# Performance work log

Measured on AMD Instinct MI355X. Metric: run time of the kernel, lower is better.

Reference implementation:

```python
import jax, jax.numpy as jnp
import numpy as np

B, C, H, W = 4, 256, 64, 64
CI = C // 2  # inter_channels


def setup_inputs() -> dict:
    key = jax.random.key(0)
    ks = jax.random.split(key, 10)
    s_in = 1.0 / np.sqrt(C)
    s_out = 1.0 / np.sqrt(CI)
    return {
        "rgbd": jax.random.normal(ks[0], (B, C, H, W), jnp.float32),
        "x": jax.random.normal(ks[1], (B, C, H, W), jnp.float32),
        "q_w": jax.random.uniform(ks[2], (CI, C), jnp.float32, -s_in, s_in),
        "q_b": jax.random.uniform(ks[3], (CI,), jnp.float32, -s_in, s_in),
        "k_w": jax.random.uniform(ks[4], (CI, C), jnp.float32, -s_in, s_in),
        "k_b": jax.random.uniform(ks[5], (CI,), jnp.float32, -s_in, s_in),
        "v_w": jax.random.uniform(ks[6], (CI, C), jnp.float32, -s_in, s_in),
        "v_b": jax.random.uniform(ks[7], (CI,), jnp.float32, -s_in, s_in),
        "out_w": jax.random.uniform(ks[8], (C, CI), jnp.float32, -s_out, s_out),
        "out_b": jax.random.uniform(ks[9], (C,), jnp.float32, -s_out, s_out),
    }


def reference(rgbd, x, q_w, q_b, k_w, k_b, v_w, v_b, out_w, out_b):
    b, c, h, w = rgbd.shape
    ci = q_w.shape[0]
    n = h * w
    # 1x1 convs == channel-wise linear maps; flatten spatial to tokens
    xs = x.reshape(b, c, n)        # [B, C, N]
    rs = rgbd.reshape(b, c, n)     # [B, C, N]
    q = jnp.einsum('oc,bcn->bno', q_w, xs) + q_b          # [B, N, CI]
    k = jnp.einsum('oc,bcn->bon', k_w, rs) + k_b[:, None]  # [B, CI, N]
    v = jnp.einsum('oc,bcn->bno', v_w, rs) + v_b          # [B, N, CI]
    attn = jax.nn.softmax(jnp.einsum('bqc,bck->bqk', q, k), axis=-1)  # [B, N, N]
    out = jnp.einsum('bqk,bkc->bqc', attn, v)             # [B, N, CI]
    out = jnp.einsum('oc,bnc->bon', out_w, out) + out_b[:, None]  # [B, C, N]
    return rgbd + out.reshape(b, c, h, w)
```

## Files before the change

### kernel.cpp

```cpp
#include <hip/hip_runtime.h>
#include <cstdint>
#include <cstddef>

typedef unsigned short u16;
typedef __attribute__((ext_vector_type(8))) short bf16x8;
typedef __attribute__((ext_vector_type(4))) float f32x4;

#define DEV __device__ __forceinline__

static constexpr float LOG2E = 1.4426950408889634f;

DEV u16 f2bf(float f) {
  uint32_t u = __float_as_uint(f);
  u += 0x7fffu + ((u >> 16) & 1u);
  return (u16)(u >> 16);
}
DEV float bf2f(u16 h) {
  uint32_t u = ((uint32_t)h) << 16;
  return __uint_as_float(u);
}
DEV uint32_t cvtpk(float lo, float hi) {
  uint32_t r;
  asm("v_cvt_pk_bf16_f32 %0, %1, %2" : "=v"(r) : "v"(lo), "v"(hi));
  return r;
}
DEV float exp2fast(float x) {
  float r;
  asm("v_exp_f32 %0, %1" : "=v"(r) : "v"(x));
  return r;
}

DEV f32x4 mfma16(bf16x8 a, bf16x8 b, f32x4 c) {
  return __builtin_amdgcn_mfma_f32_16x16x32_bf16(a, b, c, 0, 0, 0);
}

DEV void gload_lds16(const void* g, void* l) {
  __builtin_amdgcn_global_load_lds(
      (const __attribute__((address_space(1))) uint32_t*)g,
      (__attribute__((address_space(3))) uint32_t*)l, 16, 0, 0);
}

static constexpr int BATCH = 4;
static constexpr int C = 256;
static constexpr int CI = 128;
static constexpr int N = 4096;
static constexpr int SPLIT = 4;
static constexpr int KPB = N / SPLIT;
static constexpr int NT = KPB / 32;

__global__ __launch_bounds__(256) void cvt_w(const float* __restrict__ a,
                                             const float* __restrict__ b,
                                             const float* __restrict__ c,
                                             const float* __restrict__ d,
                                             u16* __restrict__ oa, u16* __restrict__ ob,
                                             u16* __restrict__ oc, u16* __restrict__ od) {
  int i = blockIdx.x * 256 + threadIdx.x;
  oa[i] = f2bf(a[i] * LOG2E);
  ob[i] = f2bf(b[i]);
  oc[i] = f2bf(c[i]);
  od[i] = f2bf(d[i]);
}

__global__ __launch_bounds__(256) void proj_kernel(
    const float* __restrict__ x, const float* __restrict__ rgbd,
    const u16* __restrict__ Wq, const u16* __restrict__ Wk, const u16* __restrict__ Wv,
    const float* __restrict__ qb, const float* __restrict__ kb, const float* __restrict__ vb,
    u16* __restrict__ Qb, u16* __restrict__ Kb, u16* __restrict__ Vtb) {
  __shared__ __align__(16) u16 xT[64][C + 8];
  __shared__ __align__(16) u16 rT[64][C + 8];
  const int b = blockIdx.y;
  const int n0 = blockIdx.x * 64;
  const int t = threadIdx.x;
  {
    const int tok = t & 63, cp = (t >> 6) * 2;
    const float* xb = x + (size_t)b * C * N + n0;
    const float* rb = rgbd + (size_t)b * C * N + n0;
    for (int c0 = 0; c0 < C; c0 += 8) {
      int c = c0 + cp;
      *(uint32_t*)&xT[tok][c] = cvtpk(xb[(size_t)c * N + tok], xb[(size_t)(c + 1) * N + tok]);
      *(uint32_t*)&rT[tok][c] = cvtpk(rb[(size_t)c * N + tok], rb[(size_t)(c + 1) * N + tok]);
    }
  }
  __syncthreads();
  const int w = t >> 6, lane = t & 63, g = lane >> 4, cl = lane & 15;

#define PROJ_QK(Sarr, W, bias, Out, SCL)                                              \
  {                                                                                   \
    bf16x8 afr[8];                                                                    \
    _Pragma("unroll") for (int ks = 0; ks < 8; ++ks)                                  \
        afr[ks] = *(const bf16x8*)&Sarr[w * 16 + cl][ks * 32 + g * 8];                \
    _Pragma("unroll") for (int ct = 0; ct < 8; ++ct) {                                \
      f32x4 acc = {0.f, 0.f, 0.f, 0.f};                                               \
      _Pragma("unroll") for (int ks = 0; ks < 8; ++ks) {                              \
        bf16x8 bb = *(const bf16x8*)&W[(size_t)(ct * 16 + cl) * C + ks * 32 + g * 8]; \
        acc = mfma16(afr[ks], bb, acc);                                               \
      }                                                                               \
      float bv = bias[ct * 16 + cl] * (SCL);                                          \
      _Pragma("unroll") for (int r = 0; r < 4; ++r) {                                 \
        int tok = n0 + w * 16 + g * 4 + r;                                            \
        Out[((size_t)b * N + tok) * CI + ct * 16 + cl] = f2bf(acc[r] + bv);           \
      }                                                                               \
    }                                                                                 \
  }

  PROJ_QK(xT, Wq, qb, Qb, LOG2E)
  PROJ_QK(rT, Wk, kb, Kb, 1.0f)
#undef PROJ_QK

  #pragma unroll
  for (int rt = 0; rt < 2; ++rt) {
    bf16x8 aw[8];
    #pragma unroll
    for (int ks = 0; ks < 8; ++ks)
      aw[ks] = *(const bf16x8*)&Wv[(size_t)(w * 32 + rt * 16 + cl) * C + ks * 32 + g * 8];
    #pragma unroll
    for (int ct = 0; ct < 4; ++ct) {
      f32x4 acc = {0.f, 0.f, 0.f, 0.f};
      #pragma unroll
      for (int ks = 0; ks < 8; ++ks) {
        bf16x8 bb = *(const bf16x8*)&rT[ct * 16 + cl][ks * 32 + g * 8];
        acc = mfma16(aw[ks], bb, acc);
      }
      #pragma unroll
      for (int r = 0; r < 4; ++r) {
        int o = w * 32 + rt * 16 + g * 4 + r;
        Vtb[((size_t)b * CI + o) * N + n0 + ct * 16 + cl] = f2bf(acc[r] + vb[o]);
      }
    }
  }
}

__global__ __launch_bounds__(256, 4) void attn_kernel(
    const u16* __restrict__ Qb, const u16* __restrict__ Kb,
    const u16* __restrict__ Vtb, u16* __restrict__ Opart,
    float2* __restrict__ ml) {
  __shared__ __align__(16) u16 Klds[2][32 * 128];
  __shared__ __align__(16) u16 Vlds[2][128 * 32];
  __shared__ __align__(16) u16 Plds[4][16][40];
  const int lin = blockIdx.x;
  const int nl = (lin & 7) * 128 + (lin >> 3);
  const int qi = nl & 63;
  const int grp = nl >> 6;
  const int b = grp & 3;
  const int s = grp >> 2;
  const int q0 = qi * 64;
  const int t = threadIdx.x;
  const int w = t >> 6, lane = t & 63, g = lane >> 4, cl = lane & 15;

  const u16* Kg = Kb + (size_t)b * N * CI;
  const u16* Vg = Vtb + (size_t)b * CI * N;

  const int k_r = t >> 4;
  const int k_ss = (t & 15) ^ k_r;
  const int v_r = t >> 2;
  const int v_ss = (t & 3) ^ ((t >> 4) & 3);
  const int wbase = (t & ~63);

#define STAGE_K(bi, k0_)                                                          \
  do {                                                                            \
    _Pragma("unroll") for (int c = 0; c < 2; ++c) {                               \
      gload_lds16(Kg + (size_t)((k0_) + c * 16 + k_r) * CI + k_ss * 8,            \
                  &Klds[bi][(c * 256 + wbase) * 8]);                              \
    }                                                                             \
  } while (0)
#define STAGE_V(bi, k0_)                                                          \
  do {                                                                            \
    _Pragma("unroll") for (int c = 0; c < 2; ++c) {                               \
      gload_lds16(Vg + (size_t)(c * 64 + v_r) * N + (k0_) + v_ss * 8,             \
                  &Vlds[bi][(c * 256 + wbase) * 8]);                              \
    }                                                                             \
  } while (0)

  const u16* Qg = Qb + ((size_t)b * N + q0 + w * 16 + cl) * CI;
  bf16x8 qf[4];
  #pragma unroll
  for (int ks = 0; ks < 4; ++ks)
    qf[ks] = *(const bf16x8*)(Qg + ks * 32 + g * 8);
  asm volatile("s_waitcnt vmcnt(0)" ::: "memory");

  f32x4 oacc[8];
  #pragma unroll
  for (int i = 0; i < 8; ++i) oacc[i] = {0.f, 0.f, 0.f, 0.f};
  float m = -1e30f, l = 0.f;

  const int kbeg = s * KPB;
  STAGE_K(0, kbeg);
  STAGE_V(0, kbeg);
  STAGE_K(1, kbeg + 32);
  STAGE_V(1, kbeg + 32);

  int buf = 0;
  for (int tt = 0; tt < NT; ++tt) {
    asm volatile("s_waitcnt vmcnt(4)" ::: "memory");
    __builtin_amdgcn_s_barrier();
    const int knext = kbeg + ((tt + 2 < NT) ? tt + 2 : tt) * 32;

    bf16x8 kf0[4], kf1[4];
    #pragma unroll
    for (int ks = 0; ks < 4; ++ks) {
      kf0[ks] = *(const bf16x8*)&Klds[buf][(cl)*128 + (((ks * 4 + g) ^ cl) & 15) * 8];
      kf1[ks] = *(const bf16x8*)&Klds[buf][(16 + cl) * 128 + (((ks * 4 + g) ^ cl) & 15) * 8];
    }
    asm volatile("s_waitcnt lgkmcnt(0)" ::: "memory");
    __builtin_amdgcn_s_barrier();
    STAGE_K(buf, knext);

    f32x4 st0 = {0.f, 0.f, 0.f, 0.f}, st1 = {0.f, 0.f, 0.f, 0.f};
    __builtin_amdgcn_s_setprio(1);
    #pragma unroll
    for (int ks = 0; ks < 4; ++ks) {
      st0 = mfma16(kf0[ks], qf[ks], st0);
      st1 = mfma16(kf1[ks], qf[ks], st1);
    }
    __builtin_amdgcn_s_setprio(0);

    float tmax = st0[0];
    #pragma unroll
    for (int r = 0; r < 4; ++r) tmax = fmaxf(tmax, st0[r]);
    #pragma unroll
    for (int r = 0; r < 4; ++r) tmax = fmaxf(tmax, st1[r]);
    tmax = fmaxf(tmax, __shfl_xor(tmax, 16));
    tmax = fmaxf(tmax, __shfl_xor(tmax, 32));
    if (!__all(tmax - m <= 11.5f)) {
      const float mn = fmaxf(m, tmax);
      const float alpha = exp2fast(m - mn);
      m = mn;
      l *= alpha;
      #pragma unroll
      for (int r = 0; r < 4; ++r) {
        float ar = __shfl(alpha, g * 4 + r);
        #pragma unroll
        for (int ct2 = 0; ct2 < 8; ++ct2) oacc[ct2][r] *= ar;
      }
    }
    float ls = 0.f;
    {
      float p0 = exp2fast(st0[0] - m), p1 = exp2fast(st0[1] - m);
      float p2 = exp2fast(st0[2] - m), p3 = exp2fast(st0[3] - m);
      ls += (p0 + p1) + (p2 + p3);
      *(uint32_t*)&Plds[w][cl][g * 4] = cvtpk(p0, p1);
      *(uint32_t*)&Plds[w][cl][g * 4 + 2] = cvtpk(p2, p3);
      p0 = exp2fast(st1[0] - m); p1 = exp2fast(st1[1] - m);
      p2 = exp2fast(st1[2] - m); p3 = exp2fast(st1[3] - m);
      ls += (p0 + p1) + (p2 + p3);
      *(uint32_t*)&Plds[w][cl][16 + g * 4] = cvtpk(p0, p1);
      *(uint32_t*)&Plds[w][cl][16 + g * 4 + 2] = cvtpk(p2, p3);
    }
    ls += __shfl_xor(ls, 16);
    ls += __shfl_xor(ls, 32);
    l += ls;
    bf16x8 pa = *(const bf16x8*)&Plds[w][cl][g * 8];

    bf16x8 vf[8];
    #pragma unroll
    for (int ct2 = 0; ct2 < 8; ++ct2)
      vf[ct2] = *(const bf16x8*)&Vlds[buf][(ct2 * 16 + cl) * 32 + ((g ^ (cl >> 2)) & 3) * 8];
    asm volatile("s_waitcnt lgkmcnt(0)" ::: "memory");
    __builtin_amdgcn_s_barrier();
    STAGE_V(buf, knext);

    __builtin_amdgcn_s_setprio(1);
    #pragma unroll
    for (int ct2 = 0; ct2 < 8; ++ct2)
      oacc[ct2] = mfma16(pa, vf[ct2], oacc[ct2]);
    __builtin_amdgcn_s_setprio(0);

    buf ^= 1;
  }
#undef STAGE_K
#undef STAGE_V

  #pragma unroll
  for (int r = 0; r < 4; ++r) {
    float lr = __shfl(l, g * 4 + r);
    float inv = 1.0f / lr;
    const int q = q0 + w * 16 + g * 4 + r;
    #pragma unroll
    for (int ct2 = 0; ct2 < 8; ++ct2)
      Opart[(((size_t)(s * BATCH + b)) * N + q) * CI + ct2 * 16 + cl] =
          f2bf(oacc[ct2][r] * inv);
  }
  if (g == 0) {
    const int q = q0 + w * 16 + cl;
    ml[(size_t)(s * BATCH + b) * N + q] = make_float2(m, l);
  }
}

template <int NS>
__global__ __launch_bounds__(256) void combine_kernel(
    const u16* __restrict__ Opart, const float2* __restrict__ ml,
    u16* __restrict__ Ob) {
  const int idx = blockIdx.x * 256 + threadIdx.x;
  const int ci8 = idx & 15;
  const int row = idx >> 4;
  float2 sv[NS];
  float M = -1e30f;
  #pragma unroll
  for (int sp = 0; sp < NS; ++sp) {
    sv[sp] = ml[(size_t)sp * BATCH * N + row];
    M = fmaxf(M, sv[sp].x);
  }
  float wv[NS], wsum = 0.f;
  #pragma unroll
  for (int sp = 0; sp < NS; ++sp) {
    wv[sp] = sv[sp].y * exp2fast(sv[sp].x - M);
    wsum += wv[sp];
  }
  const float invL = 1.0f / wsum;
  float acc[8];
  #pragma unroll
  for (int j = 0; j < 8; ++j) acc[j] = 0.f;
  #pragma unroll
  for (int sp = 0; sp < NS; ++sp) {
    const float ws = wv[sp] * invL;
    bf16x8 v = *(const bf16x8*)&Opart[((size_t)sp * BATCH * N + row) * CI + ci8 * 8];
    #pragma unroll
    for (int j = 0; j < 8; ++j) acc[j] += ws * bf2f((u16)v[j]);
  }
  bf16x8 o;
  #pragma unroll
  for (int j = 0; j < 8; ++j) o[j] = (short)f2bf(acc[j]);
  *(bf16x8*)&Ob[(size_t)row * CI + ci8 * 8] = o;
}

__global__ __launch_bounds__(256) void outproj_kernel(
    const u16* __restrict__ Ob, const u16* __restrict__ Wo,
    const float* __restrict__ obias, const float* __restrict__ rgbd,
    float* __restrict__ out) {
  const int b = blockIdx.y;
  const int n0 = blockIdx.x * 64;
  const int t = threadIdx.x;
  const int w = t >> 6, lane = t & 63, g = lane >> 4, cl = lane & 15;

  f32x4 acc[4][4];
  #pragma unroll
  for (int i = 0; i < 4; ++i)
    #pragma unroll
    for (int j = 0; j < 4; ++j) acc[i][j] = {0.f, 0.f, 0.f, 0.f};

  #pragma unroll
  for (int ks = 0; ks < 4; ++ks) {
    bf16x8 bo[4];
    #pragma unroll
    for (int ct = 0; ct < 4; ++ct)
      bo[ct] = *(const bf16x8*)&Ob[((size_t)b * N + n0 + ct * 16 + cl) * CI + ks * 32 + g * 8];
    #pragma unroll
    for (int rt = 0; rt < 4; ++rt) {
      bf16x8 aw = *(const bf16x8*)&Wo[(size_t)(w * 64 + rt * 16 + cl) * CI + ks * 32 + g * 8];
      #pragma unroll
      for (int ct = 0; ct < 4; ++ct) acc[rt][ct] = mfma16(aw, bo[ct], acc[rt][ct]);
    }
  }
  #pragma unroll
  for (int rt = 0; rt < 4; ++rt) {
    #pragma unroll
    for (int r = 0; r < 4; ++r) {
      const int o = w * 64 + rt * 16 + g * 4 + r;
      const float bb = obias[o];
      #pragma unroll
      for (int ct = 0; ct < 4; ++ct) {
        size_t idx = ((size_t)b * C + o) * N + n0 + ct * 16 + cl;
        out[idx] = rgbd[idx] + bb + acc[rt][ct][r];
      }
    }
  }
}

extern "C" void kernel_launch(void* const* d_in, const int* in_sizes, int n_in,
                              void* d_out, int out_size, void* d_ws, size_t ws_size,
                              hipStream_t stream) {
  (void)in_sizes; (void)n_in; (void)out_size; (void)ws_size;
  const float* rgbd = (const float*)d_in[0];
  const float* x    = (const float*)d_in[1];
  const float* q_w  = (const float*)d_in[2];
  const float* q_b  = (const float*)d_in[3];
  const float* k_w  = (const float*)d_in[4];
  const float* k_b  = (const float*)d_in[5];
  const float* v_w  = (const float*)d_in[6];
  const float* v_b  = (const float*)d_in[7];
  const float* o_w  = (const float*)d_in[8];
  const float* o_b  = (const float*)d_in[9];
  float* out = (float*)d_out;

  char* ws = (char*)d_ws;
  const size_t MB = 1024 * 1024;
  const size_t szQKV = (size_t)BATCH * N * CI * sizeof(u16);
  u16* Qb  = (u16*)(ws);
  u16* Kb  = (u16*)(ws + szQKV);
  u16* Vtb = (u16*)(ws + 2 * szQKV);
  u16* Wq  = (u16*)(ws + 3 * szQKV);
  u16* Wk  = Wq + (size_t)CI * C;
  u16* Wv  = Wk + (size_t)CI * C;
  u16* Wo  = Wv + (size_t)CI * C;
  u16* Opart = (u16*)(ws + 13 * MB);
  float2* ml = (float2*)(ws + 29 * MB);
  u16* Ob  = Qb;

  const int grid_attn = 64 * BATCH * SPLIT;

  cvt_w<<<dim3((C * CI) / 256), 256, 0, stream>>>(q_w, k_w, v_w, o_w, Wq, Wk, Wv, Wo);
  proj_kernel<<<dim3(N / 64, BATCH), 256, 0, stream>>>(x, rgbd, Wq, Wk, Wv,
                                                       q_b, k_b, v_b, Qb, Kb, Vtb);
  attn_kernel<<<dim3(grid_attn), 256, 0, stream>>>(Qb, Kb, Vtb, Opart, ml);
  combine_kernel<SPLIT><<<dim3(BATCH * N * (CI / 8) / 256), 256, 0, stream>>>(Opart, ml, Ob);
  outproj_kernel<<<dim3(N / 64, BATCH), 256, 0, stream>>>(Ob, Wo, o_b, rgbd, out);
}
```

Baseline: 106.6 us.

## Switch attention to 32x32x16 MFMA with register-resident P via permlane swap

Rewrites the flash-attention inner loop to use 32x32x16 bf16 MFMAs, with each wave owning 32 queries instead of 16. The block's query tile grows from 64 to 128 and the grid halves. Probabilities are packed and rearranged into the A operand in registers with v_permlane32_swap, removing the per-tile LDS round trip for P. This also halves K/V LDS traffic per query. The cost is more registers per thread (occupancy hint lowered from 4 to 2 blocks per CU) and fewer blocks to fill the GPU.

```diff
diff --git a/kernel.cpp b/kernel.cpp
--- a/kernel.cpp
+++ b/kernel.cpp
@@ -5,6 +5,8 @@
 typedef unsigned short u16;
 typedef __attribute__((ext_vector_type(8))) short bf16x8;
 typedef __attribute__((ext_vector_type(4))) float f32x4;
+typedef __attribute__((ext_vector_type(16))) float f32x16;
+typedef __attribute__((ext_vector_type(4))) uint32_t u32x4;
 
 #define DEV __device__ __forceinline__
 
@@ -29,9 +31,15 @@
   asm("v_exp_f32 %0, %1" : "=v"(r) : "v"(x));
   return r;
 }
+DEV void plswap(uint32_t& a, uint32_t& b) {
+  asm("v_permlane32_swap_b32 %0, %1" : "+v"(a), "+v"(b));
+}
 
 DEV f32x4 mfma16(bf16x8 a, bf16x8 b, f32x4 c) {
   return __builtin_amdgcn_mfma_f32_16x16x32_bf16(a, b, c, 0, 0, 0);
+}
+DEV f32x16 mfma32(bf16x8 a, bf16x8 b, f32x16 c) {
+  return __builtin_amdgcn_mfma_f32_32x32x16_bf16(a, b, c, 0, 0, 0);
 }
 
 DEV void gload_lds16(const void* g, void* l) {
@@ -130,22 +138,22 @@
   }
 }
 
-__global__ __launch_bounds__(256, 4) void attn_kernel(
+__global__ __launch_bounds__(256, 2) void attn_kernel(
     const u16* __restrict__ Qb, const u16* __restrict__ Kb,
     const u16* __restrict__ Vtb, u16* __restrict__ Opart,
     float2* __restrict__ ml) {
   __shared__ __align__(16) u16 Klds[2][32 * 128];
   __shared__ __align__(16) u16 Vlds[2][128 * 32];
-  __shared__ __align__(16) u16 Plds[4][16][40];
   const int lin = blockIdx.x;
-  const int nl = (lin & 7) * 128 + (lin >> 3);
-  const int qi = nl & 63;
-  const int grp = nl >> 6;
+  const int nl = (lin & 7) * 64 + (lin >> 3);
+  const int qi = nl & 31;
+  const int grp = nl >> 5;
   const int b = grp & 3;
   const int s = grp >> 2;
-  const int q0 = qi * 64;
+  const int q0 = qi * 128;
   const int t = threadIdx.x;
-  const int w = t >> 6, lane = t & 63, g = lane >> 4, cl = lane & 15;
+  const int w = t >> 6, lane = t & 63;
+  const int hi = lane >> 5, l31 = lane & 31;
 
   const u16* Kg = Kb + (size_t)b * N * CI;
   const u16* Vg = Vtb + (size_t)b * CI * N;
@@ -153,7 +161,7 @@
   const int k_r = t >> 4;
   const int k_ss = (t & 15) ^ k_r;
   const int v_r = t >> 2;
-  const int v_ss = (t & 3) ^ ((t >> 4) & 3);
+  const int v_ss = (t & 3) ^ ((t >> 3) & 3);
   const int wbase = (t & ~63);
 
 #define STAGE_K(bi, k0_)                                                          \
@@ -171,17 +179,19 @@
     }                                                                             \
   } while (0)
 
-  const u16* Qg = Qb + ((size_t)b * N + q0 + w * 16 + cl) * CI;
-  bf16x8 qf[4];
-  #pragma unroll
-  for (int ks = 0; ks < 4; ++ks)
-    qf[ks] = *(const bf16x8*)(Qg + ks * 32 + g * 8);
+  const u16* Qg = Qb + ((size_t)b * N + q0 + w * 32 + l31) * CI;
+  bf16x8 qf[8];
+  #pragma unroll
+  for (int mm = 0; mm < 8; ++mm)
+    qf[mm] = *(const bf16x8*)(Qg + mm * 16 + hi * 8);
   asm volatile("s_waitcnt vmcnt(0)" ::: "memory");
 
-  f32x4 oacc[8];
-  #pragma unroll
-  for (int i = 0; i < 8; ++i) oacc[i] = {0.f, 0.f, 0.f, 0.f};
-  float m = -1e30f, l = 0.f;
+  f32x16 oacc[4];
+  #pragma unroll
+  for (int ct = 0; ct < 4; ++ct)
+    #pragma unroll
+    for (int i = 0; i < 16; ++i) oacc[ct][i] = 0.f;
+  float m_run = -1e30f, l_run = 0.f;
 
   const int kbeg = s * KPB;
   STAGE_K(0, kbeg);
@@ -195,94 +205,101 @@
     __builtin_amdgcn_s_barrier();
     const int knext = kbeg + ((tt + 2 < NT) ? tt + 2 : tt) * 32;
 
-    bf16x8 kf0[4], kf1[4];
-    #pragma unroll
-    for (int ks = 0; ks < 4; ++ks) {
-      kf0[ks] = *(const bf16x8*)&Klds[buf][(cl)*128 + (((ks * 4 + g) ^ cl) & 15) * 8];
-      kf1[ks] = *(const bf16x8*)&Klds[buf][(16 + cl) * 128 + (((ks * 4 + g) ^ cl) & 15) * 8];
-    }
+    bf16x8 kf[8];
+    #pragma unroll
+    for (int mm = 0; mm < 8; ++mm)
+      kf[mm] = *(const bf16x8*)&Klds[buf][l31 * 128 + ((((mm << 1) | hi) ^ l31) & 15) * 8];
     asm volatile("s_waitcnt lgkmcnt(0)" ::: "memory");
     __builtin_amdgcn_s_barrier();
     STAGE_K(buf, knext);
 
-    f32x4 st0 = {0.f, 0.f, 0.f, 0.f}, st1 = {0.f, 0.f, 0.f, 0.f};
+    f32x16 st;
+    #pragma unroll
+    for (int i = 0; i < 16; ++i) st[i] = 0.f;
     __builtin_amdgcn_s_setprio(1);
     #pragma unroll
-    for (int ks = 0; ks < 4; ++ks) {
-      st0 = mfma16(kf0[ks], qf[ks], st0);
-      st1 = mfma16(kf1[ks], qf[ks], st1);
-    }
+    for (int mm = 0; mm < 8; ++mm) st = mfma32(kf[mm], qf[mm], st);
     __builtin_amdgcn_s_setprio(0);
 
-    float tmax = st0[0];
-    #pragma unroll
-    for (int r = 0; r < 4; ++r) tmax = fmaxf(tmax, st0[r]);
-    #pragma unroll
-    for (int r = 0; r < 4; ++r) tmax = fmaxf(tmax, st1[r]);
-    tmax = fmaxf(tmax, __shfl_xor(tmax, 16));
+    float tmax = st[0];
+    #pragma unroll
+    for (int i = 1; i < 16; ++i) tmax = fmaxf(tmax, st[i]);
     tmax = fmaxf(tmax, __shfl_xor(tmax, 32));
-    if (!__all(tmax - m <= 11.5f)) {
-      const float mn = fmaxf(m, tmax);
-      const float alpha = exp2fast(m - mn);
-      m = mn;
-      l *= alpha;
-      #pragma unroll
-      for (int r = 0; r < 4; ++r) {
-        float ar = __shfl(alpha, g * 4 + r);
-        #pragma unroll
-        for (int ct2 = 0; ct2 < 8; ++ct2) oacc[ct2][r] *= ar;
+    if (!__all(tmax - m_run <= 11.5f)) {
+      const float mn = fmaxf(m_run, tmax);
+      const float alpha = exp2fast(m_run - mn);
+      m_run = mn;
+      l_run *= alpha;
+      #pragma unroll
+      for (int reg = 0; reg < 16; ++reg) {
+        float ar = __shfl(alpha, (reg & 3) + 8 * (reg >> 2) + 4 * hi);
+        oacc[0][reg] *= ar; oacc[1][reg] *= ar;
+        oacc[2][reg] *= ar; oacc[3][reg] *= ar;
       }
     }
+    float p[16];
     float ls = 0.f;
-    {
-      float p0 = exp2fast(st0[0] - m), p1 = exp2fast(st0[1] - m);
-      float p2 = exp2fast(st0[2] - m), p3 = exp2fast(st0[3] - m);
-      ls += (p0 + p1) + (p2 + p3);
-      *(uint32_t*)&Plds[w][cl][g * 4] = cvtpk(p0, p1);
-      *(uint32_t*)&Plds[w][cl][g * 4 + 2] = cvtpk(p2, p3);
-      p0 = exp2fast(st1[0] - m); p1 = exp2fast(st1[1] - m);
-      p2 = exp2fast(st1[2] - m); p3 = exp2fast(st1[3] - m);
-      ls += (p0 + p1) + (p2 + p3);
-      *(uint32_t*)&Plds[w][cl][16 + g * 4] = cvtpk(p0, p1);
-      *(uint32_t*)&Plds[w][cl][16 + g * 4 + 2] = cvtpk(p2, p3);
-    }
-    ls += __shfl_xor(ls, 16);
+    #pragma unroll
+    for (int i = 0; i < 16; ++i) {
+      p[i] = exp2fast(st[i] - m_run);
+      ls += p[i];
+    }
     ls += __shfl_xor(ls, 32);
-    l += ls;
-    bf16x8 pa = *(const bf16x8*)&Plds[w][cl][g * 8];
-
-    bf16x8 vf[8];
-    #pragma unroll
-    for (int ct2 = 0; ct2 < 8; ++ct2)
-      vf[ct2] = *(const bf16x8*)&Vlds[buf][(ct2 * 16 + cl) * 32 + ((g ^ (cl >> 2)) & 3) * 8];
+    l_run += ls;
+
+    uint32_t d0 = cvtpk(p[0], p[1]),  e0 = cvtpk(p[4], p[5]);
+    uint32_t d1 = cvtpk(p[2], p[3]),  e1 = cvtpk(p[6], p[7]);
+    uint32_t d2 = cvtpk(p[8], p[9]),  e2 = cvtpk(p[12], p[13]);
+    uint32_t d3 = cvtpk(p[10], p[11]), e3 = cvtpk(p[14], p[15]);
+    plswap(d0, e0);
+    plswap(d1, e1);
+    plswap(d2, e2);
+    plswap(d3, e3);
+    u32x4 pw0 = {d0, d1, e0, e1};
+    u32x4 pw1 = {d2, d3, e2, e3};
+    bf16x8 pa0 = __builtin_bit_cast(bf16x8, pw0);
+    bf16x8 pa1 = __builtin_bit_cast(bf16x8, pw1);
+
+    bf16x8 vf[4][2];
+    const int vsw = (l31 >> 1) & 3;
+    #pragma unroll
+    for (int ct = 0; ct < 4; ++ct)
+      #pragma unroll
+      for (int ks = 0; ks < 2; ++ks)
+        vf[ct][ks] = *(const bf16x8*)
+            &Vlds[buf][(32 * ct + l31) * 32 + ((((ks << 1) | hi) ^ vsw) & 3) * 8];
     asm volatile("s_waitcnt lgkmcnt(0)" ::: "memory");
     __builtin_amdgcn_s_barrier();
     STAGE_V(buf, knext);
 
     __builtin_amdgcn_s_setprio(1);
     #pragma unroll
-    for (int ct2 = 0; ct2 < 8; ++ct2)
-      oacc[ct2] = mfma16(pa, vf[ct2], oacc[ct2]);
+    for (int ct = 0; ct < 4; ++ct) {
+      oacc[ct] = mfma32(pa0, vf[ct][0], oacc[ct]);
+      oacc[ct] = mfma32(pa1, vf[ct][1], oacc[ct]);
+    }
     __builtin_amdgcn_s_setprio(0);
 
     buf ^= 1;
   }
 #undef STAGE_K
 #undef STAGE_V
-
-  #pragma unroll
-  for (int r = 0; r < 4; ++r) {
-    float lr = __shfl(l, g * 4 + r);
-    float inv = 1.0f / lr;
-    const int q = q0 + w * 16 + g * 4 + r;
-    #pragma unroll
-    for (int ct2 = 0; ct2 < 8; ++ct2)
-      Opart[(((size_t)(s * BATCH + b)) * N + q) * CI + ct2 * 16 + cl] =
-          f2bf(oacc[ct2][r] * inv);
-  }
-  if (g == 0) {
-    const int q = q0 + w * 16 + cl;
-    ml[(size_t)(s * BATCH + b) * N + q] = make_float2(m, l);
+  asm volatile("s_waitcnt vmcnt(0)" ::: "memory");
+
+  const float inv = 1.0f / l_run;
+  #pragma unroll
+  for (int reg = 0; reg < 16; ++reg) {
+    const int ql = (reg & 3) + 8 * (reg >> 2) + 4 * hi;
+    const float invr = __shfl(inv, ql);
+    const int q = q0 + w * 32 + ql;
+    #pragma unroll
+    for (int ct = 0; ct < 4; ++ct)
+      Opart[(((size_t)(s * BATCH + b)) * N + q) * CI + 32 * ct + l31] =
+          f2bf(oacc[ct][reg] * invr);
+  }
+  if (lane < 32) {
+    const int q = q0 + w * 32 + lane;
+    ml[(size_t)(s * BATCH + b) * N + q] = make_float2(m_run, l_run);
   }
 }
 
@@ -396,7 +413,7 @@
   float2* ml = (float2*)(ws + 29 * MB);
   u16* Ob  = Qb;
 
-  const int grid_attn = 64 * BATCH * SPLIT;
+  const int grid_attn = 32 * BATCH * SPLIT;
 
   cvt_w<<<dim3((C * CI) / 256), 256, 0, stream>>>(q_w, k_w, v_w, o_w, Wq, Wk, Wv, Wo);
   proj_kernel<<<dim3(N / 64, BATCH), 256, 0, stream>>>(x, rgbd, Wq, Wk, Wv,
```

After: 94.85 us. 1.12x faster.
